# Kernel tuning notes

Hardware: AMD Instinct MI355X
Metric: run time of the kernel (lower is better)

Reference implementation:

```python
import jax, jax.numpy as jnp
import numpy as np

D_MODEL = 1024
N_HEADS = 16
HEAD_DIM = D_MODEL // N_HEADS  # d_keys = d_values = 64
EPS = 1e-10


def setup_inputs() -> dict:
    key = jax.random.key(0)
    ks = jax.random.split(key, 11)
    N, L, S = 4, 4096, 4096
    inp = {
        'queries': jax.random.normal(ks[0], (N, L, D_MODEL), jnp.float32),
        'keys': jax.random.normal(ks[1], (N, S, D_MODEL), jnp.float32),
        'values': jax.random.normal(ks[2], (N, S, D_MODEL), jnp.float32),
        # Dense layer params (glorot-ish scale)
        'Wq': jax.random.normal(ks[3], (D_MODEL, D_MODEL), jnp.float32) / np.sqrt(D_MODEL),
        'bq': jnp.zeros((D_MODEL,), jnp.float32),
        'Wk': jax.random.normal(ks[4], (D_MODEL, D_MODEL), jnp.float32) / np.sqrt(D_MODEL),
        'bk': jnp.zeros((D_MODEL,), jnp.float32),
        'Wv': jax.random.normal(ks[5], (D_MODEL, D_MODEL), jnp.float32) / np.sqrt(D_MODEL),
        'bv': jnp.zeros((D_MODEL,), jnp.float32),
        'Wo': jax.random.normal(ks[6], (D_MODEL, D_MODEL), jnp.float32) / np.sqrt(D_MODEL),
        'bo': jnp.zeros((D_MODEL,), jnp.float32),
    }
    return inp


def _feat(x):
    # elu(x) + 1 feature map (strictly positive)
    return jax.nn.elu(x) + 1.0


def reference(queries, keys, values, Wq, bq, Wk, bk, Wv, bv, Wo, bo):
    N, L, _ = queries.shape
    S = keys.shape[1]
    H, Dh = N_HEADS, HEAD_DIM
    # projections -> [n, l, h, d]
    Q = (queries @ Wq + bq).reshape(N, L, H, Dh)
    K = (keys @ Wk + bk).reshape(N, S, H, Dh)
    V = (values @ Wv + bv).reshape(N, S, H, Dh)
    Q_lin = _feat(Q)
    K_lin = _feat(K)
    # normalizer Z: [n, l, h]
    K_sum = K_lin.sum(axis=1)  # [n, h, d]
    Z = 1.0 / (jnp.einsum('nlhd,nhd->nlh', Q_lin, K_sum) + EPS)
    # KV outer-product accumulation: [n, h, m, d]
    KV = jnp.einsum('nshd,nshm->nhmd', K_lin, V)
    # attention output: [n, l, h, m]
    V_lin = jnp.einsum('nlhd,nhmd,nlh->nlhm', Q_lin, KV, Z)
    new_values = V_lin.reshape(N, L, H * Dh)
    return new_values @ Wo + bo
```

## Files before the change

kernel.cpp:

```cpp
#include <hip/hip_runtime.h>
#include <hip/hip_bf16.h>
#include <stdint.h>

#define D_MODEL 1024
#define NHEADS  16
#define DH      64
#define NBATCH  4
#define SEQLEN  4096
#define MROWS   (NBATCH*SEQLEN)
#define EPSV    1e-10f

typedef __hip_bfloat16 bf16;
typedef unsigned short ushort_t;
typedef __attribute__((ext_vector_type(8))) short short8;
typedef __attribute__((ext_vector_type(4))) float f32x4;

struct __align__(8) bf16x4s { bf16 a, b, c, d; };

__device__ __forceinline__ void async_copy16(void* lds, const void* g) {
  __builtin_amdgcn_global_load_lds(
      (const __attribute__((address_space(1))) unsigned int*)(uintptr_t)g,
      (__attribute__((address_space(3))) unsigned int*)(uintptr_t)lds,
      16, 0, 0);
}

__device__ __forceinline__ short f2bf_bits(float v) {
  bf16 b = __float2bfloat16(v);
  short s; __builtin_memcpy(&s, &b, 2); return s;
}
__device__ __forceinline__ float bfbits_to_f(ushort_t u) {
  return __uint_as_float(((unsigned int)u) << 16);
}

__global__ __launch_bounds__(256)
void cvt_bf16(const float* __restrict__ s, bf16* __restrict__ d) {
  const int i = blockIdx.x * 256 + threadIdx.x;
  const f32x4 v = ((const f32x4*)s)[i];
  bf16x4s o;
  o.a = __float2bfloat16(v[0]);
  o.b = __float2bfloat16(v[1]);
  o.c = __float2bfloat16(v[2]);
  o.d = __float2bfloat16(v[3]);
  ((bf16x4s*)d)[i] = o;
}

__global__ void transpose4(const float* __restrict__ s0, const float* __restrict__ s1,
                           const float* __restrict__ s2, const float* __restrict__ s3,
                           bf16* __restrict__ d0, bf16* __restrict__ d1,
                           bf16* __restrict__ d2, bf16* __restrict__ d3) {
  const float* s; bf16* d;
  switch (blockIdx.z) {
    case 0: s = s0; d = d0; break;
    case 1: s = s1; d = d1; break;
    case 2: s = s2; d = d2; break;
    default: s = s3; d = d3; break;
  }
  __shared__ float tile[32][33];
  int x = blockIdx.x*32 + threadIdx.x;
  int y = blockIdx.y*32 + threadIdx.y;
  tile[threadIdx.y][threadIdx.x] = s[(size_t)y*D_MODEL + x];
  __syncthreads();
  int xo = blockIdx.y*32 + threadIdx.x;
  int yo = blockIdx.x*32 + threadIdx.y;
  d[(size_t)yo*D_MODEL + xo] = __float2bfloat16(tile[threadIdx.x][threadIdx.y]);
}

__device__ __forceinline__ void storeC(float* p, float v) { *p = v; }
__device__ __forceinline__ void storeC(bf16*  p, float v) { *p = __float2bfloat16(v); }

template<int ACT, typename CT>
__global__ __launch_bounds__(512, 4)
void gemm_bias_act(const bf16* __restrict__ A, const bf16* __restrict__ BT,
                   const float* __restrict__ bias, CT* __restrict__ C,
                   int M, int N, int K) {
  __shared__ __align__(16) short Asm[2][128*32];
  __shared__ __align__(16) short Bsm[2][256*32];
  const int tid  = threadIdx.x;
  const int wave = tid >> 6;
  const int lane = tid & 63;

  const int nbx = N >> 8;
  const int nwg = (M >> 7) * nbx;
  int fid = blockIdx.y * nbx + blockIdx.x;
  fid = (fid & 7) * (nwg >> 3) + (fid >> 3);
  const int m0 = (fid / nbx) * 128;
  const int n0 = (fid % nbx) * 256;

  const int wr = wave >> 2, wc = wave & 3;
  const int srow = tid >> 2;
  const int ldst = (tid & 3) * 8;
  const int sgrp = ((tid & 3) ^ ((srow >> 1) & 3)) * 8;
  const int fr   = lane & 15;
  const int quad = lane >> 4;
  const int sslot = (quad ^ ((fr >> 1) & 3)) * 8;

  f32x4 acc[4][4] = {};
  const int nk = K / 32;

  async_copy16(&Asm[0][srow*32 + ldst], A + (size_t)(m0+srow)*K + sgrp);
  #pragma unroll
  for (int r = 0; r < 2; ++r) {
    const int row = r*128 + srow;
    async_copy16(&Bsm[0][row*32 + ldst], BT + (size_t)(n0+row)*K + sgrp);
  }

  int cur = 0;
  for (int t = 0; t < nk; ++t) {
    if (t + 1 < nk) {
      const int k0n = (t + 1) * 32;
      async_copy16(&Asm[cur^1][srow*32 + ldst], A + (size_t)(m0+srow)*K + k0n + sgrp);
      #pragma unroll
      for (int r = 0; r < 2; ++r) {
        const int row = r*128 + srow;
        async_copy16(&Bsm[cur^1][row*32 + ldst], BT + (size_t)(n0+row)*K + k0n + sgrp);
      }
      asm volatile("s_waitcnt vmcnt(3)" ::: "memory");
    } else {
      asm volatile("s_waitcnt vmcnt(0)" ::: "memory");
    }
    asm volatile("s_barrier" ::: "memory");

    short8 afr[4], bfr[4];
    #pragma unroll
    for (int i = 0; i < 4; ++i)
      afr[i] = *(const short8*)&Asm[cur][(wr*64 + i*16 + fr)*32 + sslot];
    #pragma unroll
    for (int j = 0; j < 4; ++j)
      bfr[j] = *(const short8*)&Bsm[cur][(wc*64 + j*16 + fr)*32 + sslot];

    __builtin_amdgcn_s_setprio(1);
    #pragma unroll
    for (int i = 0; i < 4; ++i)
      #pragma unroll
      for (int j = 0; j < 4; ++j)
        acc[i][j] = __builtin_amdgcn_mfma_f32_16x16x32_bf16(afr[i], bfr[j], acc[i][j], 0, 0, 0);
    __builtin_amdgcn_s_setprio(0);

    asm volatile("s_barrier" ::: "memory");
    cur ^= 1;
  }

  #pragma unroll
  for (int j = 0; j < 4; ++j) {
    const int gn = n0 + wc*64 + j*16 + fr;
    const float bv = bias[gn];
    #pragma unroll
    for (int i = 0; i < 4; ++i) {
      const int gm = m0 + wr*64 + i*16 + quad*4;
      #pragma unroll
      for (int r2 = 0; r2 < 4; ++r2) {
        float v = acc[i][j][r2] + bv;
        if (ACT) v = (v > 0.f) ? (v + 1.f) : __expf(v);
        storeC(&C[(size_t)(gm + r2)*N + gn], v);
      }
    }
  }
}

#define KV_SPLIT 16
__global__ __launch_bounds__(256)
void kv_kernel(const bf16* __restrict__ Kl, const bf16* __restrict__ V,
               float* __restrict__ KVp, float* __restrict__ Ksp) {
  const int b  = blockIdx.x;
  const int sp = b & (KV_SPLIT-1);
  const int nh = b >> 4;
  const int h = nh & (NHEADS-1), n = nh >> 4;
  const int tid = threadIdx.x;
  const int wave = tid >> 6, lane = tid & 63;
  const int fr = lane & 15, quad = lane >> 4;
  const int d = lane;

  __shared__ __align__(16) short Kt[64*64];
  __shared__ __align__(16) short Vt[64*64];
  __shared__ float Ksl[4][64];

  const ushort_t* Kg = (const ushort_t*)Kl;
  const ushort_t* Vg = (const ushort_t*)V;

  f32x4 acc[4] = {};
  float ksacc = 0.f;
  const int s_base = sp * (SEQLEN / KV_SPLIT);

  for (int c0 = 0; c0 < 256; c0 += 64) {
    __syncthreads();
    #pragma unroll
    for (int i = 0; i < 2; ++i) {
      const int s8 = wave*2 + i;
      const size_t gbase = ((size_t)(n*SEQLEN + s_base + c0 + s8*8))*D_MODEL + h*DH + d;
      short8 pk, pv;
      #pragma unroll
      for (int e = 0; e < 8; ++e) {
        const ushort_t ku = Kg[gbase + (size_t)e*D_MODEL];
        const ushort_t vu = Vg[gbase + (size_t)e*D_MODEL];
        pk[e] = (short)ku;
        pv[e] = (short)vu;
        ksacc += bfbits_to_f(ku);
      }
      const int wofs = d*64 + ((s8 ^ (d & 7)) << 3);
      *(short8*)&Kt[wofs] = pk;
      *(short8*)&Vt[wofs] = pv;
    }
    __syncthreads();
    #pragma unroll
    for (int k0 = 0; k0 < 2; ++k0) {
      const int s8a = k0*4 + quad;
      const int arow = wave*16 + fr;
      const short8 afr = *(const short8*)&Vt[arow*64 + ((s8a ^ (arow & 7)) << 3)];
      #pragma unroll
      for (int j = 0; j < 4; ++j) {
        const int brow = j*16 + fr;
        const short8 bfr = *(const short8*)&Kt[brow*64 + ((s8a ^ (brow & 7)) << 3)];
        acc[j] = __builtin_amdgcn_mfma_f32_16x16x32_bf16(afr, bfr, acc[j], 0, 0, 0);
      }
    }
  }

  Ksl[wave][d] = ksacc;
  __syncthreads();
  if (tid < 64)
    Ksp[b*64 + tid] = Ksl[0][tid] + Ksl[1][tid] + Ksl[2][tid] + Ksl[3][tid];

  float* outp = KVp + (size_t)b*4096;
  #pragma unroll
  for (int j = 0; j < 4; ++j)
    #pragma unroll
    for (int r = 0; r < 4; ++r)
      outp[(wave*16 + quad*4 + r)*64 + j*16 + fr] = acc[j][r];
}

__global__ __launch_bounds__(256)
void kv_reduce(const float* __restrict__ KVp, const float* __restrict__ Ksp,
               float* __restrict__ KV, float* __restrict__ Ksum) {
  const int c  = blockIdx.x;
  const int nh = blockIdx.y;
  const int e = c*1024 + threadIdx.x*4;
  f32x4 s = {};
  #pragma unroll
  for (int sp = 0; sp < KV_SPLIT; ++sp)
    s += *(const f32x4*)(KVp + ((size_t)(nh*KV_SPLIT + sp))*4096 + e);
  *(f32x4*)(KV + (size_t)nh*4096 + e) = s;
  if (c == 0 && threadIdx.x < 64) {
    float ks = 0.f;
    #pragma unroll
    for (int sp = 0; sp < KV_SPLIT; ++sp)
      ks += Ksp[(nh*KV_SPLIT + sp)*64 + threadIdx.x];
    Ksum[nh*64 + threadIdx.x] = ks;
  }
}

__device__ __forceinline__ int bswz(int row, int d) {
  return row*64 + ((((d >> 3) ^ (row & 7)) << 3) | (d & 7));
}

__global__ __launch_bounds__(256)
void vlin_kernel(const bf16* __restrict__ Ql, const float* __restrict__ KV,
                 const float* __restrict__ Ksum, bf16* __restrict__ Vl) {
  const int lc = blockIdx.x;
  const int nh = blockIdx.y;
  const int h = nh & (NHEADS-1), n = nh >> 4;
  const int tid = threadIdx.x, wave = tid >> 6, lane = tid & 63;
  const int fr = lane & 15, quad = lane >> 4;

  __shared__ __align__(16) short Bs[144*64];
  __shared__ float Zs[128];

  const float* kvp = KV + (size_t)nh*DH*DH;
  for (int i = tid; i < DH*DH; i += 256) {
    const int m = i >> 6, d = i & 63;
    const float v = kvp[i];
    const short hi = f2bf_bits(v);
    bf16 hb; __builtin_memcpy(&hb, &hi, 2);
    const short lo = f2bf_bits(v - __bfloat162float(hb));
    Bs[bswz(m, d)]      = hi;
    Bs[bswz(64 + m, d)] = lo;
  }
  if (tid < 64) {
    const float v = Ksum[nh*DH + tid];
    const short hi = f2bf_bits(v);
    bf16 hb; __builtin_memcpy(&hb, &hi, 2);
    const short lo = f2bf_bits(v - __bfloat162float(hb));
    Bs[bswz(128, tid)] = hi;
    Bs[bswz(129, tid)] = lo;
  }
  for (int i = tid; i < 14*64; i += 256)
    Bs[(130 + (i >> 6))*64 + (i & 63)] = 0;
  __syncthreads();

  const int l0 = lc * 128;
  const size_t qbase = ((size_t)(n*SEQLEN) + l0)*D_MODEL + h*DH;
  short8 afr[2][2];
  #pragma unroll
  for (int i = 0; i < 2; ++i)
    #pragma unroll
    for (int ks = 0; ks < 2; ++ks)
      afr[i][ks] = *(const short8*)(Ql + qbase +
                     (size_t)(wave*32 + i*16 + fr)*D_MODEL + ks*32 + quad*8);

  f32x4 acc[2][9] = {};
  #pragma unroll
  for (int ks = 0; ks < 2; ++ks) {
    #pragma unroll
    for (int j = 0; j < 9; ++j) {
      const int brow = j*16 + fr;
      const short8 bfr = *(const short8*)&Bs[brow*64 +
                            (((ks*4 + quad) ^ (fr & 7)) << 3)];
      #pragma unroll
      for (int i = 0; i < 2; ++i)
        acc[i][j] = __builtin_amdgcn_mfma_f32_16x16x32_bf16(afr[i][ks], bfr, acc[i][j], 0, 0, 0);
    }
  }

  #pragma unroll
  for (int i = 0; i < 2; ++i) {
    #pragma unroll
    for (int r2 = 0; r2 < 4; ++r2) {
      const float v = acc[i][8][r2];
      const float vp = v + __shfl_xor(v, 1, 64);
      if (fr == 0) Zs[wave*32 + i*16 + quad*4 + r2] = 1.0f / (vp + EPSV);
    }
  }
  __syncthreads();

  #pragma unroll
  for (int i = 0; i < 2; ++i) {
    #pragma unroll
    for (int r2 = 0; r2 < 4; ++r2) {
      const int rloc = wave*32 + i*16 + quad*4 + r2;
      const float z = Zs[rloc];
      #pragma unroll
      for (int j = 0; j < 4; ++j) {
        const float num = acc[i][j][r2] + acc[i][4 + j][r2];
        Vl[qbase + (size_t)rloc*D_MODEL + j*16 + fr] = __float2bfloat16(num * z);
      }
    }
  }
}

extern "C" void kernel_launch(void* const* d_in, const int* in_sizes, int n_in,
                              void* d_out, int out_size, void* d_ws, size_t ws_size,
                              hipStream_t stream) {
  const float* q  = (const float*)d_in[0];
  const float* k  = (const float*)d_in[1];
  const float* v  = (const float*)d_in[2];
  const float* Wq = (const float*)d_in[3];
  const float* bq = (const float*)d_in[4];
  const float* Wk = (const float*)d_in[5];
  const float* bk = (const float*)d_in[6];
  const float* Wv = (const float*)d_in[7];
  const float* bv = (const float*)d_in[8];
  const float* Wo = (const float*)d_in[9];
  const float* bo = (const float*)d_in[10];
  float* out = (float*)d_out;

  bf16* WqT = (bf16*)d_ws;
  bf16* WkT = WqT + (size_t)D_MODEL*D_MODEL;
  bf16* WvT = WkT + (size_t)D_MODEL*D_MODEL;
  bf16* WoT = WvT + (size_t)D_MODEL*D_MODEL;
  bf16* Xb  = WoT + (size_t)D_MODEL*D_MODEL;
  bf16* Ql  = Xb  + (size_t)MROWS*D_MODEL;
  bf16* Kl  = Ql  + (size_t)MROWS*D_MODEL;
  bf16* Vb  = Kl  + (size_t)MROWS*D_MODEL;
  bf16* Vl  = Kl;
  float* KV = (float*)(Vb + (size_t)MROWS*D_MODEL);
  float* Ks = KV + (size_t)NBATCH*NHEADS*DH*DH;
  float* KVp = (float*)Xb;
  float* Ksp = KVp + (size_t)NBATCH*NHEADS*KV_SPLIT*DH*DH;

  transpose4<<<dim3(32,32,4), dim3(32,32,1), 0, stream>>>(Wq,Wk,Wv,Wo, WqT,WkT,WvT,WoT);

  const int nconv4 = MROWS*D_MODEL/4;
  dim3 gb(512), gg(D_MODEL/256, MROWS/128);

  cvt_bf16<<<nconv4/256, 256, 0, stream>>>(q, Xb);
  gemm_bias_act<1,bf16><<<gg, gb, 0, stream>>>(Xb, WqT, bq, Ql, MROWS, D_MODEL, D_MODEL);
  cvt_bf16<<<nconv4/256, 256, 0, stream>>>(k, Xb);
  gemm_bias_act<1,bf16><<<gg, gb, 0, stream>>>(Xb, WkT, bk, Kl, MROWS, D_MODEL, D_MODEL);
  cvt_bf16<<<nconv4/256, 256, 0, stream>>>(v, Xb);
  gemm_bias_act<0,bf16><<<gg, gb, 0, stream>>>(Xb, WvT, bv, Vb, MROWS, D_MODEL, D_MODEL);

  kv_kernel<<<dim3(NBATCH*NHEADS*KV_SPLIT), dim3(256), 0, stream>>>(Kl, Vb, KVp, Ksp);
  kv_reduce<<<dim3(4, NBATCH*NHEADS), dim3(256), 0, stream>>>(KVp, Ksp, KV, Ks);
  vlin_kernel<<<dim3(SEQLEN/128, NBATCH*NHEADS), dim3(256), 0, stream>>>(Ql, KV, Ks, Vl);

  gemm_bias_act<0,float><<<gg, gb, 0, stream>>>(Vl, WoT, bo, out, MROWS, D_MODEL, D_MODEL);
}
```

Baseline: 448.1 us.

## Store K/V projections transposed; move KV bf16 split into reduce kernel

The K and V projection GEMMs now write their outputs transposed (feature-major), so kv_kernel can load MFMA fragments straight from global memory without LDS staging or barriers. The K column sum is now computed with an MFMA against a ones vector. kv_reduce writes the hi/lo bf16 split of KV and Ksum once per head, so vlin_kernel reads its B operand from global memory instead of rebuilding it in LDS in every block, and the Z normalizer uses a shuffle instead of LDS and a barrier. The trade-off is that the transposed epilogue writes short strided 8-byte chunks, which may make the K and V GEMM stores less efficient.

Result: slower. 475.8 us (+6.2%).

```diff
diff --git a/kernel.cpp b/kernel.cpp
--- a/kernel.cpp
+++ b/kernel.cpp
@@ -22,14 +22,6 @@
       (const __attribute__((address_space(1))) unsigned int*)(uintptr_t)g,
       (__attribute__((address_space(3))) unsigned int*)(uintptr_t)lds,
       16, 0, 0);
-}
-
-__device__ __forceinline__ short f2bf_bits(float v) {
-  bf16 b = __float2bfloat16(v);
-  short s; __builtin_memcpy(&s, &b, 2); return s;
-}
-__device__ __forceinline__ float bfbits_to_f(ushort_t u) {
-  return __uint_as_float(((unsigned int)u) << 16);
 }
 
 __global__ __launch_bounds__(256)
@@ -68,7 +60,7 @@
 __device__ __forceinline__ void storeC(float* p, float v) { *p = v; }
 __device__ __forceinline__ void storeC(bf16*  p, float v) { *p = __float2bfloat16(v); }
 
-template<int ACT, typename CT>
+template<int ACT, int TRANS, typename CT>
 __global__ __launch_bounds__(512, 4)
 void gemm_bias_act(const bf16* __restrict__ A, const bf16* __restrict__ BT,
                    const float* __restrict__ bias, CT* __restrict__ C,
@@ -147,11 +139,24 @@
     #pragma unroll
     for (int i = 0; i < 4; ++i) {
       const int gm = m0 + wr*64 + i*16 + quad*4;
-      #pragma unroll
-      for (int r2 = 0; r2 < 4; ++r2) {
-        float v = acc[i][j][r2] + bv;
-        if (ACT) v = (v > 0.f) ? (v + 1.f) : __expf(v);
-        storeC(&C[(size_t)(gm + r2)*N + gn], v);
+      if (TRANS) {
+        float vv[4];
+        #pragma unroll
+        for (int r2 = 0; r2 < 4; ++r2) {
+          float v = acc[i][j][r2] + bv;
+          if (ACT) v = (v > 0.f) ? (v + 1.f) : __expf(v);
+          vv[r2] = v;
+        }
+        bf16x4s o{__float2bfloat16(vv[0]), __float2bfloat16(vv[1]),
+                  __float2bfloat16(vv[2]), __float2bfloat16(vv[3])};
+        *(bf16x4s*)((bf16*)C + (size_t)gn*M + gm) = o;
+      } else {
+        #pragma unroll
+        for (int r2 = 0; r2 < 4; ++r2) {
+          float v = acc[i][j][r2] + bv;
+          if (ACT) v = (v > 0.f) ? (v + 1.f) : __expf(v);
+          storeC(&C[(size_t)(gm + r2)*N + gn], v);
+        }
       }
     }
   }
@@ -159,133 +164,98 @@
 
 #define KV_SPLIT 16
 __global__ __launch_bounds__(256)
-void kv_kernel(const bf16* __restrict__ Kl, const bf16* __restrict__ V,
+void kv_kernel(const bf16* __restrict__ KT, const bf16* __restrict__ VT,
                float* __restrict__ KVp, float* __restrict__ Ksp) {
   const int b  = blockIdx.x;
   const int sp = b & (KV_SPLIT-1);
   const int nh = b >> 4;
   const int h = nh & (NHEADS-1), n = nh >> 4;
   const int tid = threadIdx.x;
-  const int wave = tid >> 6, lane = tid & 63;
+  const int w = tid >> 6, lane = tid & 63;
   const int fr = lane & 15, quad = lane >> 4;
-  const int d = lane;
-
-  __shared__ __align__(16) short Kt[64*64];
-  __shared__ __align__(16) short Vt[64*64];
-  __shared__ float Ksl[4][64];
-
-  const ushort_t* Kg = (const ushort_t*)Kl;
-  const ushort_t* Vg = (const ushort_t*)V;
+
+  const size_t cbase = (size_t)n*SEQLEN + sp*(SEQLEN/KV_SPLIT);
+  const bf16* KTh = KT + (size_t)(h*DH)*MROWS + cbase;
+  const bf16* VTh = VT + (size_t)(h*DH)*MROWS + cbase;
 
   f32x4 acc[4] = {};
-  float ksacc = 0.f;
-  const int s_base = sp * (SEQLEN / KV_SPLIT);
-
-  for (int c0 = 0; c0 < 256; c0 += 64) {
-    __syncthreads();
-    #pragma unroll
-    for (int i = 0; i < 2; ++i) {
-      const int s8 = wave*2 + i;
-      const size_t gbase = ((size_t)(n*SEQLEN + s_base + c0 + s8*8))*D_MODEL + h*DH + d;
-      short8 pk, pv;
-      #pragma unroll
-      for (int e = 0; e < 8; ++e) {
-        const ushort_t ku = Kg[gbase + (size_t)e*D_MODEL];
-        const ushort_t vu = Vg[gbase + (size_t)e*D_MODEL];
-        pk[e] = (short)ku;
-        pv[e] = (short)vu;
-        ksacc += bfbits_to_f(ku);
-      }
-      const int wofs = d*64 + ((s8 ^ (d & 7)) << 3);
-      *(short8*)&Kt[wofs] = pk;
-      *(short8*)&Vt[wofs] = pv;
-    }
-    __syncthreads();
-    #pragma unroll
-    for (int k0 = 0; k0 < 2; ++k0) {
-      const int s8a = k0*4 + quad;
-      const int arow = wave*16 + fr;
-      const short8 afr = *(const short8*)&Vt[arow*64 + ((s8a ^ (arow & 7)) << 3)];
-      #pragma unroll
-      for (int j = 0; j < 4; ++j) {
-        const int brow = j*16 + fr;
-        const short8 bfr = *(const short8*)&Kt[brow*64 + ((s8a ^ (brow & 7)) << 3)];
-        acc[j] = __builtin_amdgcn_mfma_f32_16x16x32_bf16(afr, bfr, acc[j], 0, 0, 0);
-      }
-    }
-  }
-
-  Ksl[wave][d] = ksacc;
-  __syncthreads();
-  if (tid < 64)
-    Ksp[b*64 + tid] = Ksl[0][tid] + Ksl[1][tid] + Ksl[2][tid] + Ksl[3][tid];
+  f32x4 ksacc[4] = {};
+  const short8 ones8 = {0x3F80,0x3F80,0x3F80,0x3F80,0x3F80,0x3F80,0x3F80,0x3F80};
+
+  #pragma unroll
+  for (int ks = 0; ks < 8; ++ks) {
+    const int sc = ks*32 + quad*8;
+    const short8 av = *(const short8*)(VTh + (size_t)(w*16 + fr)*MROWS + sc);
+    #pragma unroll
+    for (int j = 0; j < 4; ++j) {
+      const short8 bk = *(const short8*)(KTh + (size_t)(j*16 + fr)*MROWS + sc);
+      acc[j] = __builtin_amdgcn_mfma_f32_16x16x32_bf16(av, bk, acc[j], 0, 0, 0);
+      if (w == 0)
+        ksacc[j] = __builtin_amdgcn_mfma_f32_16x16x32_bf16(ones8, bk, ksacc[j], 0, 0, 0);
+    }
+  }
 
   float* outp = KVp + (size_t)b*4096;
   #pragma unroll
   for (int j = 0; j < 4; ++j)
     #pragma unroll
     for (int r = 0; r < 4; ++r)
-      outp[(wave*16 + quad*4 + r)*64 + j*16 + fr] = acc[j][r];
+      outp[(w*16 + quad*4 + r)*64 + j*16 + fr] = acc[j][r];
+
+  if (tid < 16)
+    #pragma unroll
+    for (int j = 0; j < 4; ++j)
+      Ksp[b*64 + j*16 + tid] = ksacc[j][0];
 }
 
 __global__ __launch_bounds__(256)
 void kv_reduce(const float* __restrict__ KVp, const float* __restrict__ Ksp,
-               float* __restrict__ KV, float* __restrict__ Ksum) {
+               bf16* __restrict__ KVb) {
   const int c  = blockIdx.x;
   const int nh = blockIdx.y;
-  const int e = c*1024 + threadIdx.x*4;
+  const int tid = threadIdx.x;
+  const int e = c*1024 + tid*4;
+  const int m = e >> 6, d = e & 63;
   f32x4 s = {};
   #pragma unroll
   for (int sp = 0; sp < KV_SPLIT; ++sp)
     s += *(const f32x4*)(KVp + ((size_t)(nh*KV_SPLIT + sp))*4096 + e);
-  *(f32x4*)(KV + (size_t)nh*4096 + e) = s;
-  if (c == 0 && threadIdx.x < 64) {
-    float ks = 0.f;
-    #pragma unroll
-    for (int sp = 0; sp < KV_SPLIT; ++sp)
-      ks += Ksp[(nh*KV_SPLIT + sp)*64 + threadIdx.x];
-    Ksum[nh*64 + threadIdx.x] = ks;
-  }
-}
-
-__device__ __forceinline__ int bswz(int row, int d) {
-  return row*64 + ((((d >> 3) ^ (row & 7)) << 3) | (d & 7));
+
+  bf16* base = KVb + (size_t)nh*(144*64);
+  bf16 h0 = __float2bfloat16(s[0]), h1 = __float2bfloat16(s[1]);
+  bf16 h2 = __float2bfloat16(s[2]), h3 = __float2bfloat16(s[3]);
+  bf16x4s hi4{h0, h1, h2, h3};
+  bf16x4s lo4{__float2bfloat16(s[0] - __bfloat162float(h0)),
+              __float2bfloat16(s[1] - __bfloat162float(h1)),
+              __float2bfloat16(s[2] - __bfloat162float(h2)),
+              __float2bfloat16(s[3] - __bfloat162float(h3))};
+  *(bf16x4s*)&base[m*64 + d]        = hi4;
+  *(bf16x4s*)&base[(64 + m)*64 + d] = lo4;
+
+  if (c == 0) {
+    if (tid < 64) {
+      float ks = 0.f;
+      #pragma unroll
+      for (int sp = 0; sp < KV_SPLIT; ++sp)
+        ks += Ksp[(nh*KV_SPLIT + sp)*64 + tid];
+      bf16 hh = __float2bfloat16(ks);
+      base[128*64 + tid] = hh;
+      base[129*64 + tid] = __float2bfloat16(ks - __bfloat162float(hh));
+    }
+    for (int i2 = tid; i2 < 14*64; i2 += 256)
+      base[130*64 + i2] = __float2bfloat16(0.0f);
+  }
 }
 
 __global__ __launch_bounds__(256)
-void vlin_kernel(const bf16* __restrict__ Ql, const float* __restrict__ KV,
-                 const float* __restrict__ Ksum, bf16* __restrict__ Vl) {
+void vlin_kernel(const bf16* __restrict__ Ql, const bf16* __restrict__ KVb,
+                 bf16* __restrict__ Vl) {
   const int lc = blockIdx.x;
   const int nh = blockIdx.y;
   const int h = nh & (NHEADS-1), n = nh >> 4;
   const int tid = threadIdx.x, wave = tid >> 6, lane = tid & 63;
   const int fr = lane & 15, quad = lane >> 4;
 
-  __shared__ __align__(16) short Bs[144*64];
-  __shared__ float Zs[128];
-
-  const float* kvp = KV + (size_t)nh*DH*DH;
-  for (int i = tid; i < DH*DH; i += 256) {
-    const int m = i >> 6, d = i & 63;
-    const float v = kvp[i];
-    const short hi = f2bf_bits(v);
-    bf16 hb; __builtin_memcpy(&hb, &hi, 2);
-    const short lo = f2bf_bits(v - __bfloat162float(hb));
-    Bs[bswz(m, d)]      = hi;
-    Bs[bswz(64 + m, d)] = lo;
-  }
-  if (tid < 64) {
-    const float v = Ksum[nh*DH + tid];
-    const short hi = f2bf_bits(v);
-    bf16 hb; __builtin_memcpy(&hb, &hi, 2);
-    const short lo = f2bf_bits(v - __bfloat162float(hb));
-    Bs[bswz(128, tid)] = hi;
-    Bs[bswz(129, tid)] = lo;
-  }
-  for (int i = tid; i < 14*64; i += 256)
-    Bs[(130 + (i >> 6))*64 + (i & 63)] = 0;
-  __syncthreads();
-
   const int l0 = lc * 128;
   const size_t qbase = ((size_t)(n*SEQLEN) + l0)*D_MODEL + h*DH;
   short8 afr[2][2];
@@ -296,14 +266,13 @@
       afr[i][ks] = *(const short8*)(Ql + qbase +
                      (size_t)(wave*32 + i*16 + fr)*D_MODEL + ks*32 + quad*8);
 
+  const bf16* bb = KVb + (size_t)nh*(144*64);
   f32x4 acc[2][9] = {};
   #pragma unroll
   for (int ks = 0; ks < 2; ++ks) {
     #pragma unroll
     for (int j = 0; j < 9; ++j) {
-      const int brow = j*16 + fr;
-      const short8 bfr = *(const short8*)&Bs[brow*64 +
-                            (((ks*4 + quad) ^ (fr & 7)) << 3)];
+      const short8 bfr = *(const short8*)(bb + (j*16 + fr)*64 + ks*32 + quad*8);
       #pragma unroll
       for (int i = 0; i < 2; ++i)
         acc[i][j] = __builtin_amdgcn_mfma_f32_16x16x32_bf16(afr[i][ks], bfr, acc[i][j], 0, 0, 0);
@@ -316,17 +285,8 @@
     for (int r2 = 0; r2 < 4; ++r2) {
       const float v = acc[i][8][r2];
       const float vp = v + __shfl_xor(v, 1, 64);
-      if (fr == 0) Zs[wave*32 + i*16 + quad*4 + r2] = 1.0f / (vp + EPSV);
-    }
-  }
-  __syncthreads();
-
-  #pragma unroll
-  for (int i = 0; i < 2; ++i) {
-    #pragma unroll
-    for (int r2 = 0; r2 < 4; ++r2) {
+      const float z = 1.0f / (__shfl(vp, lane & 48, 64) + EPSV);
       const int rloc = wave*32 + i*16 + quad*4 + r2;
-      const float z = Zs[rloc];
       #pragma unroll
       for (int j = 0; j < 4; ++j) {
         const float num = acc[i][j][r2] + acc[i][4 + j][r2];
@@ -361,8 +321,7 @@
   bf16* Kl  = Ql  + (size_t)MROWS*D_MODEL;
   bf16* Vb  = Kl  + (size_t)MROWS*D_MODEL;
   bf16* Vl  = Kl;
-  float* KV = (float*)(Vb + (size_t)MROWS*D_MODEL);
-  float* Ks = KV + (size_t)NBATCH*NHEADS*DH*DH;
+  bf16* KVb = Vb + (size_t)MROWS*D_MODEL;
   float* KVp = (float*)Xb;
   float* Ksp = KVp + (size_t)NBATCH*NHEADS*KV_SPLIT*DH*DH;
 
@@ -372,15 +331,15 @@
   dim3 gb(512), gg(D_MODEL/256, MROWS/128);
 
   cvt_bf16<<<nconv4/256, 256, 0, stream>>>(q, Xb);
-  gemm_bias_act<1,bf16><<<gg, gb, 0, stream>>>(Xb, WqT, bq, Ql, MROWS, D_MODEL, D_MODEL);
+  gemm_bias_act<1,0,bf16><<<gg, gb, 0, stream>>>(Xb, WqT, bq, Ql, MROWS, D_MODEL, D_MODEL);
   cvt_bf16<<<nconv4/256, 256, 0, stream>>>(k, Xb);
-  gemm_bias_act<1,bf16><<<gg, gb, 0, stream>>>(Xb, WkT, bk, Kl, MROWS, D_MODEL, D_MODEL);
+  gemm_bias_act<1,1,bf16><<<gg, gb, 0, stream>>>(Xb, WkT, bk, Kl, MROWS, D_MODEL, D_MODEL);
   cvt_bf16<<<nconv4/256, 256, 0, stream>>>(v, Xb);
-  gemm_bias_act<0,bf16><<<gg, gb, 0, stream>>>(Xb, WvT, bv, Vb, MROWS, D_MODEL, D_MODEL);
+  gemm_bias_act<0,1,bf16><<<gg, gb, 0, stream>>>(Xb, WvT, bv, Vb, MROWS, D_MODEL, D_MODEL);
 
   kv_kernel<<<dim3(NBATCH*NHEADS*KV_SPLIT), dim3(256), 0, stream>>>(Kl, Vb, KVp, Ksp);
-  kv_reduce<<<dim3(4, NBATCH*NHEADS), dim3(256), 0, stream>>>(KVp, Ksp, KV, Ks);
-  vlin_kernel<<<dim3(SEQLEN/128, NBATCH*NHEADS), dim3(256), 0, stream>>>(Ql, KV, Ks, Vl);
-
-  gemm_bias_act<0,float><<<gg, gb, 0, stream>>>(Vl, WoT, bo, out, MROWS, D_MODEL, D_MODEL);
-}
+  kv_reduce<<<dim3(4, NBATCH*NHEADS), dim3(256), 0, stream>>>(KVp, Ksp, KVb);
+  vlin_kernel<<<dim3(SEQLEN/128, NBATCH*NHEADS), dim3(256), 0, stream>>>(Ql, KVb, Vl);
+
+  gemm_bias_act<0,0,float><<<gg, gb, 0, stream>>>(Vl, WoT, bo, out, MROWS, D_MODEL, D_MODEL);
+}
```
